# Optimization experiments

Measured on AMD Instinct MI355X. Metric: run time of the kernel, lower is better.

Reference implementation:

```python
import jax, jax.numpy as jnp
import numpy as np

EPS = 1e-5


def conv3d(x, w):
    # x: [N, C, D, H, W], w: [O, I, kD, kH, kW]; SAME padding emulates the
    # densified coordinate-expanding sparse conv on a fixed grid.
    return jax.lax.conv_general_dilated(
        x, w, window_strides=(1, 1, 1), padding='SAME',
        dimension_numbers=('NCDHW', 'OIDHW', 'NCDHW'))


def bn(x, gamma, beta, mean, var):
    # eval-mode batchnorm, fused scale/shift
    scale = gamma * jax.lax.rsqrt(var + EPS)          # [C]
    shift = beta - mean * scale                       # [C]
    return x * scale[None, :, None, None, None] + shift[None, :, None, None, None]


def setup_inputs() -> dict:
    key = jax.random.key(0)
    ks = jax.random.split(key, 20)
    C = 16
    D, H, W = 128, 128, 16

    def w(k, shape, fan):
        return jax.random.normal(k, shape, dtype=jnp.float32) / np.sqrt(fan)

    inp = {}
    inp['x'] = jax.random.normal(ks[0], (1, C, D, H, W), dtype=jnp.float32)
    inp['w1'] = w(ks[1], (C, C, 3, 3, 1), C * 9)
    inp['w2'] = w(ks[2], (C, C, 3, 3, 1), C * 9)
    inp['w3'] = w(ks[3], (C, C, 5, 5, 3), C * 75)
    inp['w4'] = w(ks[4], (C, C, 7, 7, 5), C * 245)
    inp['w5'] = w(ks[5], (C, C, 3, 3, 1), C * 9)
    inp['w6'] = w(ks[6], (C, C, 5, 5, 3), C * 75)
    inp['w7'] = w(ks[7], (C, C, 7, 7, 5), C * 245)
    inp['wch'] = w(ks[8], (C, C, 1, 1, 1), C)
    inp['wr1'] = w(ks[9], (C, C, 3, 3, 1), C * 9)
    inp['wr2'] = w(ks[10], (C, C, 5, 5, 3), C * 75)
    inp['wr3'] = w(ks[11], (C, C, 7, 7, 5), C * 245)
    # 10 BN layers: bn_1..bn_7 -> rows 0..6, bn_res_1..3 -> rows 7..9
    inp['bn_gamma'] = jax.random.uniform(ks[12], (10, C), dtype=jnp.float32) + 0.5
    inp['bn_beta'] = 0.1 * jax.random.normal(ks[13], (10, C), dtype=jnp.float32)
    inp['bn_mean'] = 0.1 * jax.random.normal(ks[14], (10, C), dtype=jnp.float32)
    inp['bn_var'] = jax.random.uniform(ks[15], (10, C), dtype=jnp.float32) + 0.5
    return inp


def reference(x, w1, w2, w3, w4, w5, w6, w7, wch, wr1, wr2, wr3,
              bn_gamma, bn_beta, bn_mean, bn_var):
    def cbn(h, w_, i):
        return bn(conv3d(h, w_), bn_gamma[i], bn_beta[i], bn_mean[i], bn_var[i])

    x1 = cbn(x, w1, 0)
    x2 = cbn(x1, w2, 1)
    x3 = cbn(x1, w3, 2)
    x4 = cbn(x1, w4, 3)
    t1 = jax.nn.relu(x2 + x3 + x4)
    x5 = cbn(t1, w5, 4)
    x6 = cbn(t1, w6, 5)
    x7 = cbn(t1, w7, 6)
    xs = jax.nn.relu(x1 + x2 + x3 + x4 + x5 + x6 + x7)
    y0 = conv3d(xs, wch)
    y1 = cbn(x, wr1, 7)
    y2 = cbn(x, wr2, 8)
    y3 = cbn(x, wr3, 9)
    return jax.nn.relu(x1 + y0 + y1 + y2 + y3)
```

## Files before the change

### kernel.cpp

```cpp
#include <hip/hip_runtime.h>
#include <hip/hip_bf16.h>

typedef __attribute__((ext_vector_type(8))) short short8;
typedef __attribute__((ext_vector_type(4))) short s16x4;
typedef __attribute__((ext_vector_type(4))) float f32x4;

constexpr int C  = 16;
constexpr int DD = 128, HH = 128, WW = 16;
constexpr int HW = HH * WW;
constexpr int SP = DD * HW;
constexpr int TOT = C * SP;

constexpr int WP_ = 20, HP_ = 134, DP_ = 134;
constexpr int ROWE   = WP_ * C;
constexpr int PLANEE = HP_ * ROWE;
constexpr int PADE   = DP_ * PLANEE;

using gas_ptr = const __attribute__((address_space(1))) void*;
using las_ptr = __attribute__((address_space(3))) void*;

constexpr int OFF_W1  = 0;
constexpr int OFF_WCH = 5 * 512;
constexpr int OFF_G0  = OFF_WCH + 512;
constexpr int OFF_G1  = OFF_G0 + 147 * 512;
constexpr int OFF_G2  = OFF_G1 + 147 * 512;
constexpr int WPK_TOT = OFF_G2 + 147 * 512;

__device__ __forceinline__ float bf16_to_f(short s)
{
    union { unsigned u; float f; } cv;
    cv.u = ((unsigned)(unsigned short)s) << 16;
    return cv.f;
}

template <int EP>
__global__ __launch_bounds__(256, 2)
void conv_tile_lds(const short* __restrict__ xp, const short* __restrict__ wpk,
                   const float* __restrict__ bias, float* __restrict__ F,
                   short* __restrict__ P)
{
    constexpr int KD = 7, KH = 7, KW = 5;
    constexpr int PH = 3;
    constexpr int KWP = 3;
    constexpr int NUP = (2 + KD - 1) / 2;
    constexpr int NB  = 8 + KH - 1;
    constexpr int NR  = 16 + 2 * PH;
    constexpr int NCHP = NR * 40;
    constexpr int NCH  = 2 * NCHP;
    constexpr int BUFSZ = 7 * 256 * 16;
    static_assert(NCH <= 7 * 256, "stage fits in 7 iterations");

    __shared__ alignas(16) char smem[2 * BUFSZ];

    const int b0   = blockIdx.x;
    const int b    = (b0 & 7) * 64 + (b0 >> 3);
    const int dblk = b >> 3, hb = b & 7;
    const int d0   = dblk * 2;
    const int tid  = threadIdx.x;
    const int wid  = tid >> 6, lane = tid & 63;
    const int pid  = wid >> 1, m = wid & 1;
    const int l15  = lane & 15;
    const int cih  = (lane >> 4) & 1;
    const int tsel = lane >> 5;

    const char* xb = (const char*)xp;
    const char* wb = (const char*)wpk;
    const int hp0  = hb * 16;

    auto stage = [&](int buf, int up) {
#pragma unroll
        for (int it = 0; it < 7; ++it) {
            int chunk = it * 256 + tid;
            int cc = chunk < NCH ? chunk : NCH - 1;
            int pl = (cc >= NCHP) ? 1 : 0;
            int cp = cc - pl * NCHP;
            const char* g = xb
                + (size_t)((d0 + 2 * up + pl) * PLANEE + hp0 * ROWE) * 2
                + (size_t)cp * 16;
            void* l = (void*)(smem + buf * BUFSZ + (it * 256 + wid * 64) * 16);
            __builtin_amdgcn_global_load_lds((gas_ptr)g, (las_ptr)l, 16, 0, 0);
        }
    };

    f32x4 acc[2][8] = {};

    stage(0, 0);
#pragma unroll 1
    for (int up = 0; up < NUP; ++up) {
        const int cur = up & 1;
        if (up + 1 < NUP) {
            stage(cur ^ 1, up + 1);
            asm volatile("s_waitcnt vmcnt(7)" ::: "memory");
        } else {
            asm volatile("s_waitcnt vmcnt(0)" ::: "memory");
        }
        __builtin_amdgcn_s_barrier();

        const int u = 2 * up + m;
        const char* lb = smem + cur * BUFSZ + m * (NR * 640) + pid * 8 * 640;
#pragma unroll
        for (int kwp = 0; kwp < KWP; ++kwp) {
            const int kwa = 2 * kwp;
            const int kwb_ = (2 * kwp + 1 < KW) ? 2 * kwp + 1 : KW - 1;
            const unsigned laneoff =
                (unsigned)((l15 + (tsel ? kwb_ : kwa)) * 32 + cih * 16);

            short8 Bf[NB];
#pragma unroll
            for (int rB = 0; rB < NB; ++rB)
                Bf[rB] = *(const short8*)(lb + rB * 640 + laneoff);
            short8 Af[2][7];
#pragma unroll
            for (int ad = 0; ad < 2; ++ad) {
                const int kd = u - ad;
                if (kd < 0 || kd >= KD) continue;
#pragma unroll
                for (int kh = 0; kh < KH; ++kh)
                    Af[ad][kh] = *(const short8*)(
                        wb + (unsigned)(((kd * KH + kh) * KWP + kwp) * 1024 + lane * 16));
            }

            __builtin_amdgcn_s_setprio(1);
#pragma unroll
            for (int ad = 0; ad < 2; ++ad) {
                const int kd = u - ad;
                if (kd < 0 || kd >= KD) continue;
#pragma unroll
                for (int kh = 0; kh < KH; ++kh) {
#pragma unroll
                    for (int r = 0; r < 8; ++r)
                        acc[ad][r] = __builtin_amdgcn_mfma_f32_16x16x32_bf16(
                            Af[ad][kh], Bf[r + kh], acc[ad][r], 0, 0, 0);
                }
            }
            __builtin_amdgcn_s_setprio(0);
        }
        __builtin_amdgcn_s_barrier();
    }

    float* mlds = (float*)smem;
    if (m == 1) {
#pragma unroll
        for (int ad = 0; ad < 2; ++ad)
#pragma unroll
            for (int r = 0; r < 8; ++r)
                *(f32x4*)&mlds[(((pid * 2 + ad) * 8 + r) * 64 + lane) * 4] = acc[ad][r];
    }
    __syncthreads();
    if (m == 1) return;
#pragma unroll
    for (int ad = 0; ad < 2; ++ad)
#pragma unroll
        for (int r = 0; r < 8; ++r) {
            const f32x4 o = *(const f32x4*)&mlds[(((pid * 2 + ad) * 8 + r) * 64 + lane) * 4];
#pragma unroll
            for (int j = 0; j < 4; ++j) acc[ad][r][j] += o[j];
        }

    const int cb = (lane >> 4) * 4;
    const f32x4 bv = *(const f32x4*)(bias + cb);
    const int h0 = hb * 16 + pid * 8;
#pragma unroll
    for (int ad = 0; ad < 2; ++ad)
#pragma unroll
        for (int r = 0; r < 8; ++r) {
            const int d = d0 + ad, h = h0 + r;
            const unsigned fidx = (unsigned)(((d * HH + h) * WW + l15) * C + cb);
            f32x4 val;
#pragma unroll
            for (int j = 0; j < 4; ++j) val[j] = acc[ad][r][j] + bv[j];
            if (EP == 0) {
                *(f32x4*)(F + fidx) = val;
            } else if (EP == 2) {
                s16x4 sv;
#pragma unroll
                for (int j = 0; j < 4; ++j) {
                    __hip_bfloat16 hv = __float2bfloat16(fmaxf(val[j], 0.f));
                    sv[j] = *(short*)&hv;
                }
                *(s16x4*)(P + (size_t)(d + 3) * PLANEE + (h + 3) * ROWE
                          + (l15 + 2) * 16 + cb) = sv;
                *(f32x4*)(F + fidx) = val;
            } else {
                const f32x4 f2 = *(const f32x4*)(F + fidx);
                short* prow = P + (size_t)(d + 3) * PLANEE + (h + 3) * ROWE
                              + (l15 + 2) * 16 + cb;
                const s16x4 xv = *(const s16x4*)prow;
                s16x4 sv;
#pragma unroll
                for (int j = 0; j < 4; ++j) {
                    const float x1 = bf16_to_f(xv[j]);
                    __hip_bfloat16 hv = __float2bfloat16(fmaxf(x1 + val[j] + f2[j], 0.f));
                    sv[j] = *(short*)&hv;
                }
                *(s16x4*)prow = sv;
            }
        }
}

template <int KD, int KH, int KW, int NTAPS, bool WF, int PW>
__global__ __launch_bounds__(256, 4)
void conv_mfma(const short* __restrict__ xp, const short* __restrict__ wpk,
               const float* __restrict__ bn_g, const float* __restrict__ bn_b,
               const float* __restrict__ bn_m, const float* __restrict__ bn_v,
               int layer, float* __restrict__ F, short* __restrict__ P)
{
    constexpr int PD = (KD - 1) / 2, PH = (KH - 1) / 2, PW_ = (KW - 1) / 2;
    constexpr int NP = (NTAPS + 1) / 2;

    const int b    = blockIdx.x;
    const int d    = b >> 3, hb = b & 7;
    const int tid  = threadIdx.x;
    const int wid  = tid >> 6, lane = tid & 63;
    const int h0   = hb * 16 + wid * 4;

    const int l15  = lane & 15;
    const int cih  = (lane >> 4) & 1;
    const int tsel = lane >> 5;
    const unsigned laneoff = (unsigned)(l15 * 32 + cih * 16);

    unsigned off_r[4];
#pragma unroll
    for (int r = 0; r < 4; ++r) {
        const int h = h0 + r;
        off_r[r] = (unsigned)((((d + (3 - PD)) * HP_ + (h + (3 - PH))) * ROWE
                               + (2 - PW_) * C) * 2) + laneoff;
    }

    const char* xb = (const char*)xp;
    const char* wb = (const char*)wpk;

    f32x4 acc[4] = {};
#pragma unroll 2
    for (int p = 0; p < NP; ++p) {
        const int ta = 2 * p;
        const int tb = (2 * p + 1 < NTAPS) ? 2 * p + 1 : NTAPS - 1;
        const int kda = ta / (KH * KW), ra = ta % (KH * KW);
        const int kha = ra / KW,        kwa = ra % KW;
        const int kdb = tb / (KH * KW), rb = tb % (KH * KW);
        const int khb = rb / KW,        kwb = rb % KW;
        const unsigned toa = (unsigned)((kda * PLANEE + kha * ROWE + kwa * C) * 2);
        const unsigned tob = (unsigned)((kdb * PLANEE + khb * ROWE + kwb * C) * 2);
        const unsigned ts  = tsel ? tob : toa;

        const short8 a = *(const short8*)(wb + (unsigned)(p * 1024 + lane * 16));
#pragma unroll
        for (int r = 0; r < 4; ++r) {
            const short8 bf = *(const short8*)(xb + (off_r[r] + ts));
            acc[r] = __builtin_amdgcn_mfma_f32_16x16x32_bf16(a, bf, acc[r], 0, 0, 0);
        }
    }

    float sc[4], sh[4];
    const int cb = (lane >> 4) * 4;
    {
        const f32x4 g  = *(const f32x4*)(bn_g + layer * C + cb);
        const f32x4 be = *(const f32x4*)(bn_b + layer * C + cb);
        const f32x4 mm = *(const f32x4*)(bn_m + layer * C + cb);
        const f32x4 v  = *(const f32x4*)(bn_v + layer * C + cb);
#pragma unroll
        for (int j = 0; j < 4; ++j) { sc[j] = g[j] / sqrtf(v[j] + 1e-5f); sh[j] = be[j] - mm[j] * sc[j]; }
    }
#pragma unroll
    for (int r = 0; r < 4; ++r) {
        const int h = h0 + r;
        f32x4 val;
#pragma unroll
        for (int j = 0; j < 4; ++j) val[j] = acc[r][j] * sc[j] + sh[j];
        if (PW == 1) {
            s16x4 sv;
#pragma unroll
            for (int j = 0; j < 4; ++j) {
                __hip_bfloat16 hv = __float2bfloat16(val[j]);
                sv[j] = *(short*)&hv;
            }
            *(s16x4*)(P + (size_t)(d + 3) * PLANEE + (h + 3) * ROWE
                      + (l15 + 2) * 16 + cb) = sv;
        }
        if (WF) {
            float* dst = F + (unsigned)(((d * HH + h) * WW + l15) * C + cb);
            *(f32x4*)dst = val;
        }
    }
}

__global__ __launch_bounds__(256, 4)
void final_conv(const short* __restrict__ xsp, const short* __restrict__ wpk,
                const float* __restrict__ F1, float* __restrict__ out)
{
    const int b    = blockIdx.x;
    const int d    = b >> 3, hb = b & 7;
    const int tid  = threadIdx.x;
    const int wid  = tid >> 6, lane = tid & 63;
    const int h0   = hb * 16 + wid * 4;
    const int l15  = lane & 15;
    const int cih  = (lane >> 4) & 1;
    const int cb   = (lane >> 4) * 4;
    const unsigned laneoff = (unsigned)((l15 + 2) * 32 + cih * 16);

    const char* xb = (const char*)xsp;
    const short8 a = *(const short8*)((const char*)wpk + (unsigned)(lane * 16));

#pragma unroll
    for (int r = 0; r < 4; ++r) {
        const int h = h0 + r;
        const unsigned off = (unsigned)(((size_t)(d + 3) * PLANEE + (h + 3) * ROWE) * 2)
                             + laneoff;
        const short8 bf = *(const short8*)(xb + off);
        f32x4 acc = {};
        acc = __builtin_amdgcn_mfma_f32_16x16x32_bf16(a, bf, acc, 0, 0, 0);
        const f32x4 f1 = *(const f32x4*)(F1 + (unsigned)(((d * HH + h) * WW + l15) * C + cb));
#pragma unroll
        for (int j = 0; j < 4; ++j) {
            const float v = fmaxf(acc[j] + f1[j], 0.f);
            out[(unsigned)((cb + j) * SP + d * HW + h * WW + l15)] = v;
        }
    }
}

__global__ __launch_bounds__(256)
void pack_x(const float* __restrict__ x, short* __restrict__ xp,
            short* __restrict__ pa)
{
    const int b  = blockIdx.x;
    const int dp = b / HP_, hp = b % HP_;
    const int t  = threadIdx.x;
    const int d  = dp - 3, h = hp - 3;
    const bool inr = ((unsigned)d < (unsigned)DD) && ((unsigned)h < (unsigned)HH);
    short* row  = xp + (unsigned)(dp * PLANEE + hp * ROWE);
    short* rowp = pa + (unsigned)(dp * PLANEE + hp * ROWE);

    const int w = t & 15, ci = t >> 4;
    float v = 0.f;
    if (inr) v = x[ci * SP + d * HW + h * WW + w];
    __hip_bfloat16 hv = __float2bfloat16(v);
    row[(w + 2) * C + ci] = *(short*)&hv;
    if (t < 64) {
        const int pi = t >> 4;
        const int wp = (pi < 2) ? pi : (16 + pi);
        row[wp * C + (t & 15)] = 0;
    }
    if (!inr) {
        for (int i = t; i < ROWE; i += 256) rowp[i] = 0;
    } else if (t < 64) {
        const int pi = t >> 4;
        const int wp = (pi < 2) ? pi : (16 + pi);
        rowp[wp * C + (t & 15)] = 0;
    }
}

__global__ __launch_bounds__(256)
void pack_small(const float* __restrict__ w1, const float* __restrict__ wch,
                short* __restrict__ dst)
{
    const int b = blockIdx.x;
    const int t = threadIdx.x;
    const int l = t >> 2, jj = t & 3;
    const int co = l & 15, cih = (l >> 4) & 1, tp = l >> 5;
    unsigned out = 0;
    if (b < 5) {
        const int tap = 2 * b + tp;
#pragma unroll
        for (int s = 0; s < 2; ++s) {
            const int ci = cih * 8 + jj * 2 + s;
            const float v = (tap < 9) ? w1[(co * C + ci) * 9 + tap] : 0.f;
            __hip_bfloat16 hv = __float2bfloat16(v);
            out |= ((unsigned)*(unsigned short*)&hv) << (16 * s);
        }
        ((unsigned*)(dst + OFF_W1))[b * 256 + l * 4 + jj] = out;
    } else {
#pragma unroll
        for (int s = 0; s < 2; ++s) {
            const int ci = cih * 8 + jj * 2 + s;
            const float v = (tp == 0) ? wch[co * C + ci] : 0.f;
            __hip_bfloat16 hv = __float2bfloat16(v);
            out |= ((unsigned)*(unsigned short*)&hv) << (16 * s);
        }
        ((unsigned*)(dst + OFF_WCH))[l * 4 + jj] = out;
    }
}

struct W9 { const float* p[9]; };

__global__ __launch_bounds__(256)
void pack_fused(W9 w, const float* __restrict__ w1,
                const float* __restrict__ bng, const float* __restrict__ bnb,
                const float* __restrict__ bnm, const float* __restrict__ bnv,
                short* __restrict__ dst, float* __restrict__ bias)
{
    constexpr int kDm[3] = {3, 5, 7}, kHm[3] = {3, 5, 7}, kWm[3] = {1, 3, 5};
    constexpr int KHWm[3] = {9, 75, 245};

    const int b = blockIdx.x;
    const int g = b / 147, pr = b % 147;
    const int row = pr / 3, kwp = pr % 3;
    const int kd = row / 7, kh = row % 7;
    const int t = threadIdx.x;
    const int l = t >> 2, jj = t & 3;
    const int co = l & 15, cih = (l >> 4) & 1, tp = l >> 5;
    const int kw = 2 * kwp + tp;

    unsigned out = 0;
#pragma unroll
    for (int s = 0; s < 2; ++s) {
        const int ci = cih * 8 + jj * 2 + s;
        float val = 0.f;
        if (kw < 5) {
#pragma unroll
            for (int m = 0; m < 3; ++m) {
                const int od = (7 - kDm[m]) / 2, oh = (7 - kHm[m]) / 2, ow = (5 - kWm[m]) / 2;
                const int rd = kd - od, rh = kh - oh, rw = kw - ow;
                if ((unsigned)rd < (unsigned)kDm[m] && (unsigned)rh < (unsigned)kHm[m]
                    && (unsigned)rw < (unsigned)kWm[m]) {
                    const int layer = g * 3 + m + 1;
                    const float sbn = bng[layer * C + co] / sqrtf(bnv[layer * C + co] + 1e-5f);
                    val += sbn * w.p[g * 3 + m][(co * C + ci) * KHWm[m]
                                               + (rd * kHm[m] + rh) * kWm[m] + rw];
                }
            }
            if (g == 2) {
                const int rd = kd - 2, rh = kh - 2, rw = kw - 2;
                if ((unsigned)rd < 3u && (unsigned)rh < 3u && rw == 0) {
                    const float sbn = bng[co] / sqrtf(bnv[co] + 1e-5f);
                    val += sbn * w1[(co * C + ci) * 9 + rd * 3 + rh];
                }
            }
        }
        __hip_bfloat16 hv = __float2bfloat16(val);
        out |= ((unsigned)*(unsigned short*)&hv) << (16 * s);
    }
    ((unsigned*)(dst + OFF_G0))[(g * 147 + pr) * 256 + l * 4 + jj] = out;

    if (pr == 0 && t < 16) {
        float bsum = 0.f;
#pragma unroll
        for (int m = 0; m < 3; ++m) {
            const int layer = g * 3 + m + 1;
            const float sbn = bng[layer * C + t] / sqrtf(bnv[layer * C + t] + 1e-5f);
            bsum += bnb[layer * C + t] - bnm[layer * C + t] * sbn;
        }
        if (g == 2) {
            const float sbn = bng[t] / sqrtf(bnv[t] + 1e-5f);
            bsum += bnb[t] - bnm[t] * sbn;
        }
        bias[g * 16 + t] = bsum;
    }
}

extern "C" void kernel_launch(void* const* d_in, const int* in_sizes, int n_in,
                              void* d_out, int out_size, void* d_ws, size_t ws_size,
                              hipStream_t stream)
{
    const float* x   = (const float*)d_in[0];
    const float* w1  = (const float*)d_in[1];
    const float* wch = (const float*)d_in[8];
    const float* bng = (const float*)d_in[12];
    const float* bnb = (const float*)d_in[13];
    const float* bnm = (const float*)d_in[14];
    const float* bnv = (const float*)d_in[15];

    W9 w9;
    w9.p[0] = (const float*)d_in[2];  w9.p[1] = (const float*)d_in[3];
    w9.p[2] = (const float*)d_in[4];  w9.p[3] = (const float*)d_in[5];
    w9.p[4] = (const float*)d_in[6];  w9.p[5] = (const float*)d_in[7];
    w9.p[6] = (const float*)d_in[9];  w9.p[7] = (const float*)d_in[10];
    w9.p[8] = (const float*)d_in[11];

    short* XP   = (short*)d_ws;
    short* PA   = XP + PADE;
    float* F1   = (float*)(PA + PADE);
    short* WPK  = (short*)(F1 + TOT);
    float* BIAS = (float*)(WPK + WPK_TOT);
    float* F2   = (float*)d_out;

    const dim3 blk(256);
    const dim3 pgrid(DP_ * HP_);
    const dim3 sgrid(DD * 8);
    const dim3 tgrid((DD / 2) * 8);

    pack_x<<<pgrid, blk, 0, stream>>>(x, XP, PA);
    pack_small<<<dim3(6), blk, 0, stream>>>(w1, wch, WPK);
    pack_fused<<<dim3(441), blk, 0, stream>>>(w9, w1, bng, bnb, bnm, bnv, WPK, BIAS);

    conv_mfma<3,3,1,9,false,1><<<sgrid, blk, 0, stream>>>(
        XP, WPK + OFF_W1, bng, bnb, bnm, bnv, 0, nullptr, PA);
    conv_tile_lds<0><<<tgrid, blk, 0, stream>>>(XP, WPK + OFF_G2, BIAS + 32, F1, nullptr);
    conv_tile_lds<2><<<tgrid, blk, 0, stream>>>(PA, WPK + OFF_G0, BIAS + 0, F2, XP);
    conv_tile_lds<3><<<tgrid, blk, 0, stream>>>(XP, WPK + OFF_G1, BIAS + 16, F2, PA);
    final_conv<<<sgrid, blk, 0, stream>>>(PA, WPK + OFF_WCH, F1, (float*)d_out);

    (void)in_sizes; (void)n_in; (void)out_size; (void)ws_size;
}
```

Baseline: 130.7 us.

## Merge independent x-branch and x1-branch big convs into one dual launch

Two independent fused big-kernel conv stages (the residual branch over x and the first branch over x1) now run in one 1024-block launch instead of two sequential 512-block launches. To do this, t1 is written into a new padded buffer T1P instead of overwriting XP, and a new pack kernel zero-initialises that buffer's padding. This is meant to remove a launch boundary and the tail idle between the two stages, filling the GPU with more concurrent blocks. It costs extra workspace and an extra padded-buffer zeroing pass, and it falls back to the old sequence if the workspace is too small.

```diff
diff --git a/kernel.cpp b/kernel.cpp
--- a/kernel.cpp
+++ b/kernel.cpp
@@ -26,6 +26,8 @@
 constexpr int OFF_G2  = OFF_G1 + 147 * 512;
 constexpr int WPK_TOT = OFF_G2 + 147 * 512;
 
+constexpr int CONV_BUFSZ = 7 * 256 * 16;
+
 __device__ __forceinline__ float bf16_to_f(short s)
 {
     union { unsigned u; float f; } cv;
@@ -34,10 +36,10 @@
 }
 
 template <int EP>
-__global__ __launch_bounds__(256, 2)
-void conv_tile_lds(const short* __restrict__ xp, const short* __restrict__ wpk,
-                   const float* __restrict__ bias, float* __restrict__ F,
-                   short* __restrict__ P)
+__device__ __forceinline__
+void conv_core(int b, const short* __restrict__ xp, const short* __restrict__ wpk,
+               const float* __restrict__ bias, float* __restrict__ F,
+               short* __restrict__ P, char* __restrict__ smem)
 {
     constexpr int KD = 7, KH = 7, KW = 5;
     constexpr int PH = 3;
@@ -47,13 +49,7 @@
     constexpr int NR  = 16 + 2 * PH;
     constexpr int NCHP = NR * 40;
     constexpr int NCH  = 2 * NCHP;
-    constexpr int BUFSZ = 7 * 256 * 16;
-    static_assert(NCH <= 7 * 256, "stage fits in 7 iterations");
-
-    __shared__ alignas(16) char smem[2 * BUFSZ];
-
-    const int b0   = blockIdx.x;
-    const int b    = (b0 & 7) * 64 + (b0 >> 3);
+
     const int dblk = b >> 3, hb = b & 7;
     const int d0   = dblk * 2;
     const int tid  = threadIdx.x;
@@ -77,7 +73,7 @@
             const char* g = xb
                 + (size_t)((d0 + 2 * up + pl) * PLANEE + hp0 * ROWE) * 2
                 + (size_t)cp * 16;
-            void* l = (void*)(smem + buf * BUFSZ + (it * 256 + wid * 64) * 16);
+            void* l = (void*)(smem + buf * CONV_BUFSZ + (it * 256 + wid * 64) * 16);
             __builtin_amdgcn_global_load_lds((gas_ptr)g, (las_ptr)l, 16, 0, 0);
         }
     };
@@ -97,7 +93,7 @@
         __builtin_amdgcn_s_barrier();
 
         const int u = 2 * up + m;
-        const char* lb = smem + cur * BUFSZ + m * (NR * 640) + pid * 8 * 640;
+        const char* lb = smem + cur * CONV_BUFSZ + m * (NR * 640) + pid * 8 * 640;
 #pragma unroll
         for (int kwp = 0; kwp < KWP; ++kwp) {
             const int kwa = 2 * kwp;
@@ -198,6 +194,36 @@
         }
 }
 
+__device__ __forceinline__ int swz512(int b0)
+{
+    return (b0 & 7) * 64 + (b0 >> 3);
+}
+
+template <int EP>
+__global__ __launch_bounds__(256, 2)
+void conv_tile_lds(const short* __restrict__ xp, const short* __restrict__ wpk,
+                   const float* __restrict__ bias, float* __restrict__ F,
+                   short* __restrict__ P)
+{
+    __shared__ alignas(16) char smem[2 * CONV_BUFSZ];
+    conv_core<EP>(swz512(blockIdx.x), xp, wpk, bias, F, P, smem);
+}
+
+__global__ __launch_bounds__(256, 2)
+void conv_dual(const short* __restrict__ xpA, const short* __restrict__ wpkA,
+               const float* __restrict__ biasA, float* __restrict__ FA,
+               short* __restrict__ PA_,
+               const short* __restrict__ xpB, const short* __restrict__ wpkB,
+               const float* __restrict__ biasB, float* __restrict__ FB)
+{
+    __shared__ alignas(16) char smem[2 * CONV_BUFSZ];
+    const int b0 = blockIdx.x;
+    if (b0 < 512)
+        conv_core<2>(swz512(b0), xpA, wpkA, biasA, FA, PA_, smem);
+    else
+        conv_core<0>(swz512(b0 - 512), xpB, wpkB, biasB, FB, nullptr, smem);
+}
+
 template <int KD, int KH, int KW, int NTAPS, bool WF, int PW>
 __global__ __launch_bounds__(256, 4)
 void conv_mfma(const short* __restrict__ xp, const short* __restrict__ wpk,
@@ -346,6 +372,39 @@
         const int pi = t >> 4;
         const int wp = (pi < 2) ? pi : (16 + pi);
         rowp[wp * C + (t & 15)] = 0;
+    }
+}
+
+__global__ __launch_bounds__(256)
+void pack_x2(const float* __restrict__ x, short* __restrict__ xp,
+             short* __restrict__ pa, short* __restrict__ t1p)
+{
+    const int b  = blockIdx.x;
+    const int dp = b / HP_, hp = b % HP_;
+    const int t  = threadIdx.x;
+    const int d  = dp - 3, h = hp - 3;
+    const bool inr = ((unsigned)d < (unsigned)DD) && ((unsigned)h < (unsigned)HH);
+    short* row  = xp  + (unsigned)(dp * PLANEE + hp * ROWE);
+    short* rowp = pa  + (unsigned)(dp * PLANEE + hp * ROWE);
+    short* rowt = t1p + (unsigned)(dp * PLANEE + hp * ROWE);
+
+    const int w = t & 15, ci = t >> 4;
+    float v = 0.f;
+    if (inr) v = x[ci * SP + d * HW + h * WW + w];
+    __hip_bfloat16 hv = __float2bfloat16(v);
+    row[(w + 2) * C + ci] = *(short*)&hv;
+    if (t < 64) {
+        const int pi = t >> 4;
+        const int wp = (pi < 2) ? pi : (16 + pi);
+        row[wp * C + (t & 15)] = 0;
+    }
+    if (!inr) {
+        for (int i = t; i < ROWE; i += 256) { rowp[i] = 0; rowt[i] = 0; }
+    } else if (t < 64) {
+        const int pi = t >> 4;
+        const int wp = (pi < 2) ? pi : (16 + pi);
+        rowp[wp * C + (t & 15)] = 0;
+        rowt[wp * C + (t & 15)] = 0;
     }
 }
 
@@ -471,22 +530,36 @@
     float* F1   = (float*)(PA + PADE);
     short* WPK  = (short*)(F1 + TOT);
     float* BIAS = (float*)(WPK + WPK_TOT);
+    short* T1P  = (short*)(BIAS + 64);
     float* F2   = (float*)d_out;
+
+    const size_t need = ((size_t)(3 * PADE + WPK_TOT) * 2)
+                      + (size_t)TOT * 4 + 64 * 4;
+    const bool merged = ws_size >= need;
 
     const dim3 blk(256);
     const dim3 pgrid(DP_ * HP_);
     const dim3 sgrid(DD * 8);
-    const dim3 tgrid((DD / 2) * 8);
-
-    pack_x<<<pgrid, blk, 0, stream>>>(x, XP, PA);
+    const dim3 tgrid(512);
+
+    if (merged) pack_x2<<<pgrid, blk, 0, stream>>>(x, XP, PA, T1P);
+    else        pack_x<<<pgrid, blk, 0, stream>>>(x, XP, PA);
     pack_small<<<dim3(6), blk, 0, stream>>>(w1, wch, WPK);
     pack_fused<<<dim3(441), blk, 0, stream>>>(w9, w1, bng, bnb, bnm, bnv, WPK, BIAS);
 
     conv_mfma<3,3,1,9,false,1><<<sgrid, blk, 0, stream>>>(
         XP, WPK + OFF_W1, bng, bnb, bnm, bnv, 0, nullptr, PA);
-    conv_tile_lds<0><<<tgrid, blk, 0, stream>>>(XP, WPK + OFF_G2, BIAS + 32, F1, nullptr);
-    conv_tile_lds<2><<<tgrid, blk, 0, stream>>>(PA, WPK + OFF_G0, BIAS + 0, F2, XP);
-    conv_tile_lds<3><<<tgrid, blk, 0, stream>>>(XP, WPK + OFF_G1, BIAS + 16, F2, PA);
+
+    if (merged) {
+        conv_dual<<<dim3(1024), blk, 0, stream>>>(
+            PA, WPK + OFF_G0, BIAS + 0, F2, T1P,
+            XP, WPK + OFF_G2, BIAS + 32, F1);
+        conv_tile_lds<3><<<tgrid, blk, 0, stream>>>(T1P, WPK + OFF_G1, BIAS + 16, F2, PA);
+    } else {
+        conv_tile_lds<0><<<tgrid, blk, 0, stream>>>(XP, WPK + OFF_G2, BIAS + 32, F1, nullptr);
+        conv_tile_lds<2><<<tgrid, blk, 0, stream>>>(PA, WPK + OFF_G0, BIAS + 0, F2, XP);
+        conv_tile_lds<3><<<tgrid, blk, 0, stream>>>(XP, WPK + OFF_G1, BIAS + 16, F2, PA);
+    }
     final_conv<<<sgrid, blk, 0, stream>>>(PA, WPK + OFF_WCH, F1, (float*)d_out);
 
     (void)in_sizes; (void)n_in; (void)out_size; (void)ws_size;
```

Measured after the change: 127.4 us (median of 2 runs). -2.5%, faster.
